# Kernel optimization log

Measured on AMD Instinct MI355X. Metric: run time of the kernel, lower is better.

Reference implementation:

```python
import jax, jax.numpy as jnp
import numpy as np


def _next_fast_len(n):
    # smallest 5-smooth integer >= n (matches scipy.fftpack.next_fast_len)
    while True:
        m = n
        for p in (2, 3, 5):
            while m % p == 0:
                m //= p
        if m == 1:
            return n
        n += 1


def _conv1d_fft(values, weights):
    # values: [b, h, n, d], weights: [h, m]; FFT cross-correlation implementing
    # causal exponentially-decaying weighted sum (per-head EMA of values).
    N = values.shape[-2]
    M = weights.shape[-1]
    L = _next_fast_len(N + M - 1)
    f_v = jnp.fft.rfft(values, n=L, axis=-2)          # [b,h,F,d] complex
    f_w = jnp.fft.rfft(weights, n=L, axis=-1)         # [h,F]   complex
    out = jnp.fft.irfft(f_v * jnp.conj(f_w)[..., None], n=L, axis=-2)
    out = jnp.roll(out, -1, axis=-2)
    return out[..., L - N:, :]                         # [b,h,N,d]


def setup_inputs() -> dict:
    key = jax.random.key(0)
    ks = jax.random.split(key, 7)
    B, N, D, H = 4, 8192, 512, 8
    s = 1.0 / np.sqrt(D)
    return {
        "x": jax.random.normal(ks[0], (B, N, D), dtype=jnp.float32),
        "W_in": jax.random.normal(ks[1], (D, D), dtype=jnp.float32) * s,
        "b_in": jax.random.normal(ks[2], (D,), dtype=jnp.float32) * 0.01,
        "W_out": jax.random.normal(ks[3], (D, D), dtype=jnp.float32) * s,
        "b_out": jax.random.normal(ks[4], (D,), dtype=jnp.float32) * 0.01,
        "init_state": jax.random.normal(ks[5], (H, D // H), dtype=jnp.float32),
        "alpha_param": jax.random.normal(ks[6], (H,), dtype=jnp.float32),
    }


def reference(x, W_in, b_in, W_out, b_out, init_state, alpha_param):
    B, N, D = x.shape
    H, Dh = init_state.shape
    # input projection
    xp = x @ W_in.T + b_in                             # [B,N,D]
    xh = xp.reshape(B, N, H, Dh).transpose(0, 2, 1, 3)  # [B,H,N,Dh]
    # prepend learned init state, take first differences along time
    x0 = jnp.broadcast_to(init_state[None, :, None, :], (B, H, 1, Dh))
    xc = jnp.concatenate([x0, xh], axis=2)             # [B,H,N+1,Dh]
    xd = xc[:, :, 1:] - xc[:, :, :-1]                  # [B,H,N,Dh]
    # per-head smoothing coefficients
    alpha = jax.nn.sigmoid(alpha_param)[:, None]       # [H,1]
    ar = jnp.arange(N, dtype=x.dtype)
    weights = alpha * (1.0 - alpha) ** ar[::-1]        # [H,N]
    out = _conv1d_fft(xd, weights)                     # [B,H,N,Dh]
    # contribution of the initial state
    init_w = (1.0 - alpha) ** (ar + 1.0)               # [H,N]
    out = out + init_w[:, :, None] * init_state[:, None, :]
    out = out.transpose(0, 2, 1, 3).reshape(B, N, D)
    return out @ W_out.T + b_out
```

## Files before the change

kernel.cpp:

```cpp
#include <hip/hip_runtime.h>
#include <stdint.h>

#define SEQ      8192
#define BATCH    4
#define DIM      512
#define MROWS    32768
#define CHUNK    64
#define NCHUNK   128
#define NCHAN    2048
#define NHEAD    8
#define NGCHUNK  512
#define XLD      264

typedef unsigned short ushort;
typedef unsigned int   uint;
typedef __bf16 bf16x8 __attribute__((ext_vector_type(8)));
typedef float  f32x4  __attribute__((ext_vector_type(4)));
typedef ushort usx8   __attribute__((ext_vector_type(8)));

__device__ __forceinline__ ushort f2bf(float f) {
    union { __bf16 h; ushort u; } cv;
    cv.h = (__bf16)f;
    return cv.u;
}
__device__ __forceinline__ float bf2f(ushort v) {
    return __uint_as_float(((unsigned)v) << 16);
}

__global__ void weights_to_bf16_kernel(const float* __restrict__ w_in,
                                       const float* __restrict__ w_out,
                                       ushort* __restrict__ dst, int n4each) {
    int i = blockIdx.x * blockDim.x + threadIdx.x;
    if (i >= 2 * n4each) return;
    const float4* src = (i < n4each) ? (const float4*)w_in
                                     : (const float4*)w_out - n4each;
    float4 v = src[i];
    ushort4 r;
    r.x = f2bf(v.x); r.y = f2bf(v.y); r.z = f2bf(v.z); r.w = f2bf(v.w);
    ((ushort4*)dst)[i] = r;
}

#define GLDS(g, l) __builtin_amdgcn_global_load_lds(                        \
        (const __attribute__((address_space(1))) void*)(g),                 \
        (__attribute__((address_space(3))) void*)(l), 16, 0, 0)

__global__ __launch_bounds__(512, 4) void gemm1_scan_kernel(
        const float* __restrict__ x,    const ushort* __restrict__ Bw,
        const float* __restrict__ b_in, const float* __restrict__ alpha_param,
        ushort* __restrict__ zout,
        float* __restrict__ Lfin,       float* __restrict__ XpT)
{
    __shared__ __align__(16) char smem[2 * XLD * 128];
    ushort* As0 = (ushort*)smem;
    ushort* Bs0 = (ushort*)(smem + 16384);
    ushort* X   = (ushort*)smem;

    const int tid = threadIdx.x;
    const int bn  = blockIdx.x;
    const int bm  = blockIdx.y;

    const int lane = tid & 63;
    const int wave = tid >> 6;
    const int wr = wave >> 2, wc = wave & 3;
    const int quad = lane >> 4, r16 = lane & 15;

    const int srow  = tid >> 2;
    const int skoff = (tid & 3) * 8;
    const float*  Ag  = x  + (size_t)(bm * 128 + srow) * DIM + skoff;
    const ushort* Bg0 = Bw + (size_t)(bn * 256 + srow) * DIM + skoff;
    const ushort* Bg1 = Bg0 + (size_t)128 * DIM;

    f32x4 acc[4][4];
    #pragma unroll
    for (int i = 0; i < 4; i++)
        #pragma unroll
        for (int j = 0; j < 4; j++)
            acc[i][j] = f32x4{0.f, 0.f, 0.f, 0.f};

    const int nIter = DIM / 32;

    auto stageB = [&](int k0, int b) {
        GLDS(Bg0 + k0, &Bs0[b * 8192 + tid * 8]);
        GLDS(Bg1 + k0, &Bs0[b * 8192 + 4096 + tid * 8]);
    };
    auto cvt8 = [&](const float* s) {
        usx8 w;
        #pragma unroll
        for (int u = 0; u < 8; u++) w[u] = f2bf(s[u]);
        return w;
    };

    stageB(0, 0);
    {
        float a[8];
        #pragma unroll
        for (int u = 0; u < 8; u++) a[u] = Ag[u];
        *(usx8*)&As0[tid * 8] = cvt8(a);
    }

    int buf = 0;
    for (int k = 0; k < nIter; ++k) {
        __syncthreads();

        float an[8];
        const bool more = (k + 1 < nIter);
        if (more) {
            const int ko = (k + 1) * 32;
            stageB(ko, buf ^ 1);
            #pragma unroll
            for (int u = 0; u < 8; u++) an[u] = Ag[ko + u];
        }

        bf16x8 af[4], bfr[4];
        #pragma unroll
        for (int i = 0; i < 4; i++)
            af[i] = *(const bf16x8*)&As0[buf * 4096 + (wr * 64 + i * 16 + r16) * 32 + quad * 8];
        #pragma unroll
        for (int j = 0; j < 4; j++)
            bfr[j] = *(const bf16x8*)&Bs0[buf * 8192 + (wc * 64 + j * 16 + r16) * 32 + quad * 8];

        #pragma unroll
        for (int i = 0; i < 4; i++)
            #pragma unroll
            for (int j = 0; j < 4; j++)
                acc[i][j] = __builtin_amdgcn_mfma_f32_16x16x32_bf16(
                                bfr[j], af[i], acc[i][j], 0, 0, 0);

        if (more)
            *(usx8*)&As0[(buf ^ 1) * 4096 + tid * 8] = cvt8(an);
        buf ^= 1;
    }

    __syncthreads();
    #pragma unroll
    for (int i = 0; i < 4; i++) {
        const int ml = wr * 64 + i * 16 + r16;
        #pragma unroll
        for (int j = 0; j < 4; j++) {
            const int nl = wc * 64 + j * 16 + quad * 4;
            const float4 bv = *(const float4*)&b_in[bn * 256 + nl];
            ushort4 r4;
            r4.x = f2bf(acc[i][j][0] + bv.x);
            r4.y = f2bf(acc[i][j][1] + bv.y);
            r4.z = f2bf(acc[i][j][2] + bv.z);
            r4.w = f2bf(acc[i][j][3] + bv.w);
            *(ushort4*)&X[ml * XLD + nl] = r4;
        }
    }
    __syncthreads();

    const int chalf = tid >> 8;
    const int cidx  = tid & 255;
    const int g     = 2 * bm + chalf;
    const int d     = bn * 256 + cidx;
    const int h     = d >> 6;
    const float alpha = 1.0f / (1.0f + expf(-alpha_param[h]));
    const float c     = 1.0f - alpha;

    const ushort* Xr  = X + chalf * 64 * XLD + cidx;
    ushort* zrow = zout + ((size_t)(bm * 128 + chalf * 64)) * DIM + d;

    float z = 0.f, prev = 0.f;
    #pragma unroll 8
    for (int r = 0; r < CHUNK; ++r) {
        float xv = bf2f(Xr[r * XLD]);
        z = c * z + alpha * (xv - prev);
        prev = xv;
        zrow[(size_t)r * DIM] = f2bf(z);
    }
    Lfin[(size_t)g * 512 + d]       = z;
    XpT[(size_t)(g + 1) * 512 + d]  = prev;
}

__global__ void scan_fixg_kernel(const float* __restrict__ Lfin,
                                 const float* __restrict__ XpT,
                                 const float* __restrict__ alpha_param,
                                 const float* __restrict__ init_state,
                                 float* __restrict__ G)
{
    int ch = blockIdx.x * blockDim.x + threadIdx.x;
    if (ch >= NCHAN) return;
    const int b = ch >> 9;
    const int d = ch & (DIM - 1);
    const int h = d >> 6;
    const float alpha = 1.0f / (1.0f + expf(-alpha_param[h]));
    const float c = 1.0f - alpha;
    const float c2 = c * c, c4 = c2 * c2, c8 = c4 * c4,
                c16 = c8 * c8, c32 = c16 * c16;
    const float c63 = c32 * c16 * c8 * c4 * c2 * c;
    const float sinit = init_state[d];

    float Z = sinit;
    const float* Lp = Lfin + (size_t)(b * NCHUNK) * 512 + d;
    const float* Xp = XpT  + (size_t)(b * NCHUNK) * 512 + d;
    float*       Gp = G    + (size_t)(b * NCHUNK) * 512 + d;

    constexpr int PF = 16;
    float Lr[PF], Xr[PF];
    #pragma unroll
    for (int j = 0; j < PF; ++j) {
        Lr[j] = Lp[(size_t)j * 512];
        Xr[j] = Xp[(size_t)j * 512];
    }
    for (int gr = 0; gr < NCHUNK / PF; ++gr) {
        #pragma unroll
        for (int j = 0; j < PF; ++j) {
            const int kl = gr * PF + j;
            const float xpt = (kl == 0) ? sinit : Xr[j];
            const float Lc  = Lr[j];
            if (gr + 1 < NCHUNK / PF) {
                Lr[j] = Lp[(size_t)((gr + 1) * PF + j) * 512];
                Xr[j] = Xp[(size_t)((gr + 1) * PF + j) * 512];
            }
            const float Gv = c * Z - alpha * xpt;
            Gp[(size_t)kl * 512] = Gv;
            Z = Lc + c63 * Gv;
        }
    }
}

__global__ __launch_bounds__(512, 4) void gemm2_kernel(
        const ushort* __restrict__ Az, const ushort* __restrict__ Bw,
        const float* __restrict__ bias, float* __restrict__ Cout,
        const float* __restrict__ G, const float* __restrict__ alpha_param)
{
    __shared__ __align__(16) ushort As[2][128 * 32];
    __shared__ __align__(16) ushort Bs[2][256 * 32];

    const int tid  = threadIdx.x;
    const int lane = tid & 63;
    const int wave = tid >> 6;
    const int wr = wave >> 2, wc = wave & 3;
    const int bm = blockIdx.y, bn = blockIdx.x;
    const int quad = lane >> 4, r16 = lane & 15;

    const int srow  = tid >> 2;
    const int skoff = (tid & 3) * 8;
    const ushort* Ag16 = Az + (size_t)(bm * 128 + srow) * DIM + skoff;
    const ushort* Bg0  = Bw + (size_t)(bn * 256 + srow) * DIM + skoff;
    const ushort* Bg1  = Bg0 + (size_t)128 * DIM;

    const int m   = bm * 128 + srow;
    const int tau = m & (CHUNK - 1);
    const float* Gc = G + (size_t)(m >> 6) * 512;
    const float t1 = (float)tau;
    float fc0,fc1,fc2,fc3,fc4,fc5,fc6,fc7;
    {
        float a, c;
        a = 1.f/(1.f+expf(-alpha_param[0])); c = 1.f - a; fc0 = exp2f(t1 * log2f(c));
        a = 1.f/(1.f+expf(-alpha_param[1])); c = 1.f - a; fc1 = exp2f(t1 * log2f(c));
        a = 1.f/(1.f+expf(-alpha_param[2])); c = 1.f - a; fc2 = exp2f(t1 * log2f(c));
        a = 1.f/(1.f+expf(-alpha_param[3])); c = 1.f - a; fc3 = exp2f(t1 * log2f(c));
        a = 1.f/(1.f+expf(-alpha_param[4])); c = 1.f - a; fc4 = exp2f(t1 * log2f(c));
        a = 1.f/(1.f+expf(-alpha_param[5])); c = 1.f - a; fc5 = exp2f(t1 * log2f(c));
        a = 1.f/(1.f+expf(-alpha_param[6])); c = 1.f - a; fc6 = exp2f(t1 * log2f(c));
        a = 1.f/(1.f+expf(-alpha_param[7])); c = 1.f - a; fc7 = exp2f(t1 * log2f(c));
    }
    auto selfac = [&](int hh) -> float {
        float f = fc0;
        f = (hh == 1) ? fc1 : f;
        f = (hh == 2) ? fc2 : f;
        f = (hh == 3) ? fc3 : f;
        f = (hh == 4) ? fc4 : f;
        f = (hh == 5) ? fc5 : f;
        f = (hh == 6) ? fc6 : f;
        f = (hh == 7) ? fc7 : f;
        return f;
    };
    auto fixpack = [&](usx8 av, float4 z0, float4 z1, float fac) {
        usx8 w;
        w[0] = f2bf(bf2f(av[0]) + fac * z0.x);
        w[1] = f2bf(bf2f(av[1]) + fac * z0.y);
        w[2] = f2bf(bf2f(av[2]) + fac * z0.z);
        w[3] = f2bf(bf2f(av[3]) + fac * z0.w);
        w[4] = f2bf(bf2f(av[4]) + fac * z1.x);
        w[5] = f2bf(bf2f(av[5]) + fac * z1.y);
        w[6] = f2bf(bf2f(av[6]) + fac * z1.z);
        w[7] = f2bf(bf2f(av[7]) + fac * z1.w);
        return w;
    };

    f32x4 acc[4][4];
    #pragma unroll
    for (int i = 0; i < 4; i++)
        #pragma unroll
        for (int j = 0; j < 4; j++)
            acc[i][j] = f32x4{0.f, 0.f, 0.f, 0.f};

    const int nIter = DIM / 32;

    auto stageB = [&](int k0, int b) {
        GLDS(Bg0 + k0, &Bs[b][tid * 8]);
        GLDS(Bg1 + k0, &Bs[b][128 * 32 + tid * 8]);
    };

    stageB(0, 0);
    {
        usx8 av = *(const usx8*)(Ag16);
        float4 z0 = *(const float4*)&Gc[skoff];
        float4 z1 = *(const float4*)&Gc[skoff + 4];
        *(usx8*)&As[0][tid * 8] = fixpack(av, z0, z1, selfac(skoff >> 6));
    }

    int buf = 0;
    for (int k = 0; k < nIter; ++k) {
        __syncthreads();

        usx8 av_n; float4 zn0, zn1; float fac_n = 0.f;
        const bool more = (k + 1 < nIter);
        if (more) {
            const int ko = (k + 1) * 32;
            stageB(ko, buf ^ 1);
            av_n = *(const usx8*)(Ag16 + ko);
            const int dbase = ko + skoff;
            zn0 = *(const float4*)&Gc[dbase];
            zn1 = *(const float4*)&Gc[dbase + 4];
            fac_n = selfac(dbase >> 6);
        }

        bf16x8 af[4], bfr[4];
        #pragma unroll
        for (int i = 0; i < 4; i++)
            af[i] = *(const bf16x8*)&As[buf][(wr * 64 + i * 16 + r16) * 32 + quad * 8];
        #pragma unroll
        for (int j = 0; j < 4; j++)
            bfr[j] = *(const bf16x8*)&Bs[buf][(wc * 64 + j * 16 + r16) * 32 + quad * 8];

        #pragma unroll
        for (int i = 0; i < 4; i++)
            #pragma unroll
            for (int j = 0; j < 4; j++)
                acc[i][j] = __builtin_amdgcn_mfma_f32_16x16x32_bf16(
                                bfr[j], af[i], acc[i][j], 0, 0, 0);

        if (more)
            *(usx8*)&As[buf ^ 1][tid * 8] = fixpack(av_n, zn0, zn1, fac_n);
        buf ^= 1;
    }

    #pragma unroll
    for (int i = 0; i < 4; i++) {
        const int mr = bm * 128 + wr * 64 + i * 16 + r16;
        #pragma unroll
        for (int j = 0; j < 4; j++) {
            const int n0 = bn * 256 + wc * 64 + j * 16 + quad * 4;
            const float4 bv = *(const float4*)&bias[n0];
            float4 v = make_float4(acc[i][j][0] + bv.x, acc[i][j][1] + bv.y,
                                   acc[i][j][2] + bv.z, acc[i][j][3] + bv.w);
            *(float4*)&Cout[(size_t)mr * DIM + n0] = v;
        }
    }
}

extern "C" void kernel_launch(void* const* d_in, const int* in_sizes, int n_in,
                              void* d_out, int out_size, void* d_ws, size_t ws_size,
                              hipStream_t stream) {
    const float* x           = (const float*)d_in[0];
    const float* W_in        = (const float*)d_in[1];
    const float* b_in        = (const float*)d_in[2];
    const float* W_out       = (const float*)d_in[3];
    const float* b_out       = (const float*)d_in[4];
    const float* init_state  = (const float*)d_in[5];
    const float* alpha_param = (const float*)d_in[6];
    float* out = (float*)d_out;

    ushort* z_bf    = (ushort*)d_ws;
    ushort* win_bf  = z_bf   + (size_t)MROWS * DIM;
    ushort* wout_bf = win_bf + (size_t)DIM * DIM;
    float*  Lfin    = (float*)(wout_bf + (size_t)DIM * DIM);
    float*  XpT     = Lfin + (size_t)NGCHUNK * 512;
    float*  G       = XpT  + (size_t)(NGCHUNK + 1) * 512;

    const int nw4 = (DIM * DIM) / 4;
    weights_to_bf16_kernel<<<(2 * nw4 + 255) / 256, 256, 0, stream>>>(
        W_in, W_out, win_bf, nw4);

    dim3 g1(2, MROWS / 128);
    gemm1_scan_kernel<<<g1, 512, 0, stream>>>(
        x, win_bf, b_in, alpha_param, z_bf, Lfin, XpT);

    scan_fixg_kernel<<<NCHAN / 256, 256, 0, stream>>>(
        Lfin, XpT, alpha_param, init_state, G);

    dim3 g2(2, MROWS / 128);
    gemm2_kernel<<<g2, 512, 0, stream>>>(
        z_bf, wout_bf, b_out, out, G, alpha_param);
}
```

Measured before the change: 196.5 us.

## Triple-buffer GEMM k-loops with explicit vmcnt waits and two-stage prefetch

Both GEMM kernels move from a double-buffered k-loop to a fully unrolled three-stage LDS ring. B tiles are prefetched two iterations ahead via global_load_lds, and A register loads alternate between two register sets. Explicit s_waitcnt vmcnt/lgkmcnt waits with raw barriers and sched_barrier replace __syncthreads, so more global-load latency can hide behind MFMA work. LDS per block grows to 72 KB, which may limit occupancy, and the hand-counted vmcnt values are fragile if the compiler reorders memory ops.

Measured after the change: 177.0 us. -9.9%, faster.

```diff
diff --git a/kernel.cpp b/kernel.cpp
--- a/kernel.cpp
+++ b/kernel.cpp
@@ -11,6 +11,7 @@
 #define NHEAD    8
 #define NGCHUNK  512
 #define XLD      264
+#define NITER    16
 
 typedef unsigned short ushort;
 typedef unsigned int   uint;
@@ -44,15 +45,21 @@
         (const __attribute__((address_space(1))) void*)(g),                 \
         (__attribute__((address_space(3))) void*)(l), 16, 0, 0)
 
+#define WAITV(n)  asm volatile("s_waitcnt vmcnt(" #n ")" ::: "memory")
+#define WAITL0()  asm volatile("s_waitcnt lgkmcnt(0)" ::: "memory")
+#define BAR()     do { __builtin_amdgcn_s_barrier();                        \
+                       __builtin_amdgcn_sched_barrier(0); } while (0)
+#define SBAR()    __builtin_amdgcn_sched_barrier(0)
+
 __global__ __launch_bounds__(512, 4) void gemm1_scan_kernel(
         const float* __restrict__ x,    const ushort* __restrict__ Bw,
         const float* __restrict__ b_in, const float* __restrict__ alpha_param,
         ushort* __restrict__ zout,
         float* __restrict__ Lfin,       float* __restrict__ XpT)
 {
-    __shared__ __align__(16) char smem[2 * XLD * 128];
+    __shared__ __align__(16) char smem[73728];
     ushort* As0 = (ushort*)smem;
-    ushort* Bs0 = (ushort*)(smem + 16384);
+    ushort* Bs0 = (ushort*)(smem + 24576);
     ushort* X   = (ushort*)smem;
 
     const int tid = threadIdx.x;
@@ -77,47 +84,57 @@
         for (int j = 0; j < 4; j++)
             acc[i][j] = f32x4{0.f, 0.f, 0.f, 0.f};
 
-    const int nIter = DIM / 32;
-
     auto stageB = [&](int k0, int b) {
         GLDS(Bg0 + k0, &Bs0[b * 8192 + tid * 8]);
         GLDS(Bg1 + k0, &Bs0[b * 8192 + 4096 + tid * 8]);
     };
-    auto cvt8 = [&](const float* s) {
+    auto packA = [&](float4 lo, float4 hi) {
         usx8 w;
-        #pragma unroll
-        for (int u = 0; u < 8; u++) w[u] = f2bf(s[u]);
+        w[0] = f2bf(lo.x); w[1] = f2bf(lo.y); w[2] = f2bf(lo.z); w[3] = f2bf(lo.w);
+        w[4] = f2bf(hi.x); w[5] = f2bf(hi.y); w[6] = f2bf(hi.z); w[7] = f2bf(hi.w);
         return w;
     };
 
+    float4 aLo0, aHi0, aLo1, aHi1;
+
+    aLo0 = *(const float4*)(Ag);      aHi0 = *(const float4*)(Ag + 4);
     stageB(0, 0);
-    {
-        float a[8];
-        #pragma unroll
-        for (int u = 0; u < 8; u++) a[u] = Ag[u];
-        *(usx8*)&As0[tid * 8] = cvt8(a);
-    }
-
-    int buf = 0;
-    for (int k = 0; k < nIter; ++k) {
-        __syncthreads();
-
-        float an[8];
-        const bool more = (k + 1 < nIter);
-        if (more) {
-            const int ko = (k + 1) * 32;
-            stageB(ko, buf ^ 1);
-            #pragma unroll
-            for (int u = 0; u < 8; u++) an[u] = Ag[ko + u];
+    aLo1 = *(const float4*)(Ag + 32); aHi1 = *(const float4*)(Ag + 36);
+    stageB(32, 1);
+    *(usx8*)&As0[tid * 8] = packA(aLo0, aHi0);
+
+    #pragma unroll
+    for (int k = 0; k < NITER; ++k) {
+        const int cur = k % 3;
+        const int stg = (k + 2) % 3;
+        const int wnx = (k + 1) % 3;
+
+        if (k + 1 < NITER) {
+            usx8 w = ((k & 1) == 0) ? packA(aLo1, aHi1) : packA(aLo0, aHi0);
+            *(usx8*)&As0[wnx * 4096 + tid * 8] = w;
+        }
+        if (k < NITER - 1) WAITV(4); else WAITV(0);
+        WAITL0();
+        BAR();
+
+        if (k + 2 < NITER) {
+            const int ko = (k + 2) * 32;
+            if ((k & 1) == 0) {
+                aLo0 = *(const float4*)(Ag + ko); aHi0 = *(const float4*)(Ag + ko + 4);
+            } else {
+                aLo1 = *(const float4*)(Ag + ko); aHi1 = *(const float4*)(Ag + ko + 4);
+            }
+            SBAR();
+            stageB(ko, stg);
         }
 
         bf16x8 af[4], bfr[4];
         #pragma unroll
         for (int i = 0; i < 4; i++)
-            af[i] = *(const bf16x8*)&As0[buf * 4096 + (wr * 64 + i * 16 + r16) * 32 + quad * 8];
+            af[i] = *(const bf16x8*)&As0[cur * 4096 + (wr * 64 + i * 16 + r16) * 32 + quad * 8];
         #pragma unroll
         for (int j = 0; j < 4; j++)
-            bfr[j] = *(const bf16x8*)&Bs0[buf * 8192 + (wc * 64 + j * 16 + r16) * 32 + quad * 8];
+            bfr[j] = *(const bf16x8*)&Bs0[cur * 8192 + (wc * 64 + j * 16 + r16) * 32 + quad * 8];
 
         #pragma unroll
         for (int i = 0; i < 4; i++)
@@ -125,10 +142,6 @@
             for (int j = 0; j < 4; j++)
                 acc[i][j] = __builtin_amdgcn_mfma_f32_16x16x32_bf16(
                                 bfr[j], af[i], acc[i][j], 0, 0, 0);
-
-        if (more)
-            *(usx8*)&As0[(buf ^ 1) * 4096 + tid * 8] = cvt8(an);
-        buf ^= 1;
     }
 
     __syncthreads();
@@ -224,8 +237,9 @@
         const float* __restrict__ bias, float* __restrict__ Cout,
         const float* __restrict__ G, const float* __restrict__ alpha_param)
 {
-    __shared__ __align__(16) ushort As[2][128 * 32];
-    __shared__ __align__(16) ushort Bs[2][256 * 32];
+    __shared__ __align__(16) char smem[73728];
+    ushort* As0 = (ushort*)smem;
+    ushort* Bs0 = (ushort*)(smem + 24576);
 
     const int tid  = threadIdx.x;
     const int lane = tid & 63;
@@ -287,44 +301,59 @@
         for (int j = 0; j < 4; j++)
             acc[i][j] = f32x4{0.f, 0.f, 0.f, 0.f};
 
-    const int nIter = DIM / 32;
-
     auto stageB = [&](int k0, int b) {
-        GLDS(Bg0 + k0, &Bs[b][tid * 8]);
-        GLDS(Bg1 + k0, &Bs[b][128 * 32 + tid * 8]);
+        GLDS(Bg0 + k0, &Bs0[b * 8192 + tid * 8]);
+        GLDS(Bg1 + k0, &Bs0[b * 8192 + 4096 + tid * 8]);
     };
 
+    usx8 av0, av1; float4 g0lo, g0hi, g1lo, g1hi;
+
+    av0 = *(const usx8*)(Ag16);
+    g0lo = *(const float4*)&Gc[skoff]; g0hi = *(const float4*)&Gc[skoff + 4];
     stageB(0, 0);
-    {
-        usx8 av = *(const usx8*)(Ag16);
-        float4 z0 = *(const float4*)&Gc[skoff];
-        float4 z1 = *(const float4*)&Gc[skoff + 4];
-        *(usx8*)&As[0][tid * 8] = fixpack(av, z0, z1, selfac(skoff >> 6));
-    }
-
-    int buf = 0;
-    for (int k = 0; k < nIter; ++k) {
-        __syncthreads();
-
-        usx8 av_n; float4 zn0, zn1; float fac_n = 0.f;
-        const bool more = (k + 1 < nIter);
-        if (more) {
-            const int ko = (k + 1) * 32;
-            stageB(ko, buf ^ 1);
-            av_n = *(const usx8*)(Ag16 + ko);
-            const int dbase = ko + skoff;
-            zn0 = *(const float4*)&Gc[dbase];
-            zn1 = *(const float4*)&Gc[dbase + 4];
-            fac_n = selfac(dbase >> 6);
+    av1 = *(const usx8*)(Ag16 + 32);
+    g1lo = *(const float4*)&Gc[32 + skoff]; g1hi = *(const float4*)&Gc[32 + skoff + 4];
+    stageB(32, 1);
+    *(usx8*)&As0[tid * 8] = fixpack(av0, g0lo, g0hi, selfac(skoff >> 6));
+
+    #pragma unroll
+    for (int k = 0; k < NITER; ++k) {
+        const int cur = k % 3;
+        const int stg = (k + 2) % 3;
+        const int wnx = (k + 1) % 3;
+
+        if (k + 1 < NITER) {
+            const float fac = selfac((((k + 1) * 32) + skoff) >> 6);
+            usx8 w = ((k & 1) == 0) ? fixpack(av1, g1lo, g1hi, fac)
+                                    : fixpack(av0, g0lo, g0hi, fac);
+            *(usx8*)&As0[wnx * 4096 + tid * 8] = w;
+        }
+        if (k < NITER - 1) WAITV(5); else WAITV(0);
+        WAITL0();
+        BAR();
+
+        if (k + 2 < NITER) {
+            const int ko = (k + 2) * 32;
+            if ((k & 1) == 0) {
+                av0 = *(const usx8*)(Ag16 + ko);
+                g0lo = *(const float4*)&Gc[ko + skoff];
+                g0hi = *(const float4*)&Gc[ko + skoff + 4];
+            } else {
+                av1 = *(const usx8*)(Ag16 + ko);
+                g1lo = *(const float4*)&Gc[ko + skoff];
+                g1hi = *(const float4*)&Gc[ko + skoff + 4];
+            }
+            SBAR();
+            stageB(ko, stg);
         }
 
         bf16x8 af[4], bfr[4];
         #pragma unroll
         for (int i = 0; i < 4; i++)
-            af[i] = *(const bf16x8*)&As[buf][(wr * 64 + i * 16 + r16) * 32 + quad * 8];
+            af[i] = *(const bf16x8*)&As0[cur * 4096 + (wr * 64 + i * 16 + r16) * 32 + quad * 8];
         #pragma unroll
         for (int j = 0; j < 4; j++)
-            bfr[j] = *(const bf16x8*)&Bs[buf][(wc * 64 + j * 16 + r16) * 32 + quad * 8];
+            bfr[j] = *(const bf16x8*)&Bs0[cur * 8192 + (wc * 64 + j * 16 + r16) * 32 + quad * 8];
 
         #pragma unroll
         for (int i = 0; i < 4; i++)
@@ -332,10 +361,6 @@
             for (int j = 0; j < 4; j++)
                 acc[i][j] = __builtin_amdgcn_mfma_f32_16x16x32_bf16(
                                 bfr[j], af[i], acc[i][j], 0, 0, 0);
-
-        if (more)
-            *(usx8*)&As[buf ^ 1][tid * 8] = fixpack(av_n, zn0, zn1, fac_n);
-        buf ^= 1;
     }
 
     #pragma unroll
```
